# Kernel tuning notes

Hardware: AMD Instinct MI355X
Metric: run time of the kernel (lower is better)

## Reference

```python
import jax, jax.numpy as jnp
import numpy as np

NEG_SLOPE = 0.2


def add_self_loops(edge_index, num_nodes):
    loop = jnp.arange(num_nodes, dtype=edge_index.dtype)
    loops = jnp.stack([loop, loop])  # [2, N]
    return jnp.concatenate([edge_index, loops], axis=1)


def gat_conv(x, edge_index, W, a_src, a_dst, b, concat=True):
    """PyG-style GATConv. a_src/a_dst: [1, H, C]. W: [F_in, H*C]."""
    N = x.shape[0]
    H, C = a_src.shape[1], a_src.shape[2]
    xp = (x @ W).reshape(N, H, C)                       # [N, H, C]
    alpha_src = (xp * a_src).sum(-1)                    # [N, H]
    alpha_dst = (xp * a_dst).sum(-1)                    # [N, H]
    src, dst = edge_index[0], edge_index[1]
    e = alpha_src[src] + alpha_dst[dst]                 # [E, H]
    e = jnp.where(e > 0, e, NEG_SLOPE * e)              # LeakyReLU(0.2)
    # per-destination segment softmax
    m = jax.ops.segment_max(e, dst, num_segments=N)     # [N, H]
    m = jnp.where(jnp.isfinite(m), m, 0.0)
    ez = jnp.exp(e - m[dst])
    s = jax.ops.segment_sum(ez, dst, num_segments=N)    # [N, H]
    alpha = ez / (s[dst] + 1e-16)                       # [E, H]
    msg = xp[src] * alpha[:, :, None]                   # [E, H, C]
    out = jax.ops.segment_sum(msg, dst, num_segments=N) # [N, H, C]
    out = out.reshape(N, H * C) if concat else out.mean(axis=1)
    return out + b


def setup_inputs() -> dict:
    key = jax.random.key(0)
    ks = jax.random.split(key, 16)
    N, F, E, CLS = 100000, 256, 1600000, 10
    x = jax.random.normal(ks[0], (N, F), dtype=jnp.float32)
    edge_index = jax.random.randint(ks[1], (2, E), 0, N, dtype=jnp.int64)

    def glorot(k, shape):
        fan = shape[0] + shape[-1] * (shape[1] if len(shape) == 3 else 1)
        return jax.random.uniform(k, shape, jnp.float32, -1.0, 1.0) * jnp.sqrt(6.0 / fan)

    return {
        "x": x, "edge_index": edge_index,
        "W1": glorot(ks[2], (F, 128)),  "a1s": glorot(ks[3], (1, 8, 16)),
        "a1d": glorot(ks[4], (1, 8, 16)), "b1": jnp.zeros((128,), jnp.float32),
        "W2": glorot(ks[5], (128, 64)), "a2s": glorot(ks[6], (1, 8, 8)),
        "a2d": glorot(ks[7], (1, 8, 8)),  "b2": jnp.zeros((64,), jnp.float32),
        "W3": glorot(ks[8], (64, CLS)), "a3s": glorot(ks[9], (1, 1, CLS)),
        "a3d": glorot(ks[10], (1, 1, CLS)), "b3": jnp.zeros((CLS,), jnp.float32),
    }


def reference(x, edge_index, W1, a1s, a1d, b1, W2, a2s, a2d, b2, W3, a3s, a3d, b3):
    ei = add_self_loops(edge_index, x.shape[0])
    h = jax.nn.elu(gat_conv(x, ei, W1, a1s, a1d, b1))
    h = jax.nn.elu(gat_conv(h, ei, W2, a2s, a2d, b2))
    h = gat_conv(h, ei, W3, a3s, a3d, b3)
    return jax.nn.log_softmax(h, axis=1)
```

## Files before the change

kernel.cpp:

```cpp
#include <hip/hip_runtime.h>
#include <hip/hip_bf16.h>
#include <math.h>


#define LEAKY(v) ((v) > 0.f ? (v) : 0.2f * (v))

typedef __bf16 bf16_t;
typedef __bf16 bf16x8 __attribute__((ext_vector_type(8)));
typedef __bf16 bf16x4 __attribute__((ext_vector_type(4)));
typedef float f32x4 __attribute__((ext_vector_type(4)));
typedef unsigned short u16x8 __attribute__((ext_vector_type(8)));

static __device__ __forceinline__ unsigned short bf_bits(float f) {
    bf16_t b = (bf16_t)f;
    return __builtin_bit_cast(unsigned short, b);
}
static __device__ __forceinline__ float bf_to_f(unsigned short u) {
    return __uint_as_float(((unsigned int)u) << 16);
}
static __device__ __forceinline__ float bperm_f(int byteaddr, float v) {
    return __uint_as_float((unsigned)__builtin_amdgcn_ds_bpermute(byteaddr, (int)__float_as_uint(v)));
}

constexpr int NB_MAX = 400;
constexpr int BCAP = 5120;

__global__ __launch_bounds__(256) void partition_k(
        const int* __restrict__ src, const int* __restrict__ dst, int E, int NB,
        int* __restrict__ bcur, unsigned* __restrict__ staged) {
    __shared__ int hist[NB_MAX];
    __shared__ int bstart[NB_MAX + 1];
    __shared__ int cur[NB_MAX];
    __shared__ int gbase[NB_MAX];
    __shared__ unsigned words[4096];
    __shared__ unsigned short bidl[4096];
    int tid = threadIdx.x;
    int e0 = blockIdx.x * 4096;
    int cnt = E - e0; if (cnt > 4096) cnt = 4096;
    if (cnt <= 0) return;

    for (int b = tid; b < NB; b += 256) hist[b] = 0;
    __syncthreads();
    for (int i = tid; i < cnt; i += 256) atomicAdd(&hist[dst[e0 + i] >> 8], 1);
    __syncthreads();
    if (tid == 0) {
        int run = 0;
        for (int b = 0; b < NB; b++) { bstart[b] = run; run += hist[b]; }
        bstart[NB] = run;
    }
    __syncthreads();
    for (int b = tid; b < NB; b += 256) {
        cur[b] = bstart[b];
        gbase[b] = hist[b] ? atomicAdd(&bcur[b], hist[b]) : 0;
    }
    __syncthreads();
    for (int i = tid; i < cnt; i += 256) {
        int s = src[e0 + i], d = dst[e0 + i];
        int b = d >> 8;
        unsigned w = (unsigned)s | ((unsigned)(d & 255) << 17);
        int p = atomicAdd(&cur[b], 1);
        words[p] = w;
        bidl[p] = (unsigned short)b;
    }
    __syncthreads();
    for (int i = tid; i < cnt; i += 256) {
        int b = bidl[i];
        staged[(size_t)b * BCAP + gbase[b] + (i - bstart[b])] = words[i];
    }
}

__global__ void scan_nb_k(const int* __restrict__ bcur, int* __restrict__ ebase, int NB) {
    int lane = threadIdx.x;
    int CH = (NB + 63) / 64;
    int b0 = lane * CH;
    int v[8]; int s = 0;
#pragma unroll 8
    for (int k = 0; k < CH; k++) { int b = b0 + k; int t = (b < NB) ? bcur[b] : 0; if (k < 8) v[k] = t; s += t; }
    int orig = s;
    for (int off = 1; off < 64; off <<= 1) {
        int t = __shfl_up(s, off, 64);
        if (lane >= off) s += t;
    }
    int run = s - orig;
    for (int k = 0; k < CH; k++) { int b = b0 + k; if (b < NB) { ebase[b] = run; run += v[k]; } }
    if (lane == 63) ebase[NB] = run;
}

__global__ __launch_bounds__(256) void buildcsr_k(
        const unsigned* __restrict__ staged, const int* __restrict__ bcur,
        const int* __restrict__ ebase, int* __restrict__ offs, int* __restrict__ cols,
        int N, int NB) {
    __shared__ int h[256], hs[256], curl[256];
    __shared__ int colsl[BCAP];
    int b = blockIdx.x, tid = threadIdx.x;
    int n0 = b << 8;
    int ecnt = bcur[b];
    int base_g = ebase[b];
    const unsigned* sb = staged + (size_t)b * BCAP;

    h[tid] = 0;
    __syncthreads();
    for (int i = tid; i < ecnt; i += 256) atomicAdd(&h[sb[i] >> 17], 1);
    __syncthreads();
    int val = h[tid];
    hs[tid] = val; __syncthreads();
    for (int off = 1; off < 256; off <<= 1) {
        int t = (tid >= off) ? hs[tid - off] : 0;
        __syncthreads();
        hs[tid] += t;
        __syncthreads();
    }
    int excl = hs[tid] - val;
    curl[tid] = excl;
    if (n0 + tid < N) offs[n0 + tid] = base_g + excl;
    if (b == NB - 1 && tid == 0) offs[N] = base_g + ecnt;
    __syncthreads();
    for (int i = tid; i < ecnt; i += 256) {
        unsigned w = sb[i];
        int p = atomicAdd(&curl[w >> 17], 1);
        colsl[p] = (int)(w & 0x1FFFFu);
    }
    __syncthreads();
    for (int i = tid; i < ecnt; i += 256) cols[base_g + i] = colsl[i];
}

__global__ void prep_w_k(const float* __restrict__ W, short* __restrict__ Bfs,
                         int K, int N, int NT, int total) {
    int idx = blockIdx.x * blockDim.x + threadIdx.x;
    if (idx >= total) return;
    int lane = idx & 63;
    int t = idx >> 6;
    int ntile = t % NT, kstep = t / NT;
    int quad = lane >> 4, nl = lane & 15;
    int n = ntile * 16 + nl;
    bf16_t* dst = (bf16_t*)Bfs + (size_t)idx * 16;
#pragma unroll
    for (int j = 0; j < 8; j++) {
        int k = kstep * 32 + quad * 8 + j;
        float v = W[k * N + n];
        bf16_t h = (bf16_t)v;
        bf16_t l = (bf16_t)(v - (float)h);
        dst[j] = h;
        dst[8 + j] = l;
    }
}

__global__ void prep_w3_k(const float* __restrict__ W, short* __restrict__ Bfs, int Nc) {
    int idx = blockIdx.x * blockDim.x + threadIdx.x;
    if (idx >= 128) return;
    int lane = idx & 63, ks = idx >> 6;
    int quad = lane >> 4, nl = lane & 15;
    bf16_t* dst = (bf16_t*)Bfs + (size_t)idx * 16;
#pragma unroll
    for (int j = 0; j < 8; j++) {
        int k = ks * 32 + quad * 8 + j;
        float v = (nl < Nc) ? W[k * Nc + nl] : 0.f;
        bf16_t h = (bf16_t)v;
        bf16_t l = (bf16_t)(v - (float)h);
        dst[j] = h;
        dst[8 + j] = l;
    }
}

template <int BM, int WMT, int WNT, int NWM, bool ABF16, int CHEAD, int K>
__global__ __launch_bounds__(256, 2) void mfma_gemm_k(
        const void* __restrict__ Av, const short* __restrict__ Bfs,
        unsigned short* __restrict__ Cb,
        const float* __restrict__ a_s, const float* __restrict__ a_d,
        float* __restrict__ out_as, float* __restrict__ out_ad,
        int M, int N, int NT) {
    constexpr int NWN = 4 / NWM;
    constexpr int BN = 16 * WNT * NWN;
    constexpr int KP = K + 8;
    __shared__ __align__(16) bf16_t As_hi[BM * KP];
    __shared__ __align__(16) bf16_t As_lo[ABF16 ? 16 : BM * KP];
    const bf16_t* Bf = (const bf16_t*)Bfs;

    int tid = threadIdx.x;
    int wave = tid >> 6, lane = tid & 63;
    int quad = lane >> 4, l16 = lane & 15;
    int wm = wave % NWM, wn = wave / NWM;
    int row0 = blockIdx.x * BM;
    int ntile0 = blockIdx.y * (BN / 16) + wn * WNT;

    if constexpr (!ABF16) {
        constexpr int CHUNKS = BM * K * 4 / (16 * 256);
        const float* A = (const float*)Av;
        f32x4 tmp[CHUNKS];
#pragma unroll
        for (int c = 0; c < CHUNKS; c++) {
            int ci = c * 256 + tid;
            int fi = ci * 4;
            int row = fi / K, k = fi % K;
            int grow = row0 + row;
            tmp[c] = (f32x4){0.f, 0.f, 0.f, 0.f};
            if (grow < M) tmp[c] = *(const f32x4*)(A + (size_t)grow * K + k);
        }
#pragma unroll
        for (int c = 0; c < CHUNKS; c++) {
            int ci = c * 256 + tid;
            int fi = ci * 4;
            int row = fi / K, k = fi % K;
            bf16x4 h, l;
#pragma unroll
            for (int j = 0; j < 4; j++) {
                bf16_t hh = (bf16_t)tmp[c][j];
                h[j] = hh;
                l[j] = (bf16_t)(tmp[c][j] - (float)hh);
            }
            *(bf16x4*)&As_hi[row * KP + k] = h;
            *(bf16x4*)&As_lo[row * KP + k] = l;
        }
    } else {
        constexpr int CHUNKS = BM * K * 2 / (16 * 256);
        const unsigned short* A = (const unsigned short*)Av;
        u16x8 tmp[CHUNKS];
#pragma unroll
        for (int c = 0; c < CHUNKS; c++) {
            int ci = c * 256 + tid;
            int ei = ci * 8;
            int row = ei / K, k = ei % K;
            int grow = row0 + row;
            tmp[c] = (u16x8){0, 0, 0, 0, 0, 0, 0, 0};
            if (grow < M) tmp[c] = *(const u16x8*)(A + (size_t)grow * K + k);
        }
#pragma unroll
        for (int c = 0; c < CHUNKS; c++) {
            int ci = c * 256 + tid;
            int ei = ci * 8;
            int row = ei / K, k = ei % K;
            *(u16x8*)&As_hi[row * KP + k] = tmp[c];
        }
    }
    __syncthreads();

    f32x4 acc[WMT][WNT];
#pragma unroll
    for (int i = 0; i < WMT; i++)
#pragma unroll
        for (int j = 0; j < WNT; j++) acc[i][j] = (f32x4){0.f, 0.f, 0.f, 0.f};

#pragma unroll
    for (int ks = 0; ks < K / 32; ks++) {
        bf16x8 ah[WMT], al[WMT];
#pragma unroll
        for (int i = 0; i < WMT; i++) {
            int rowl = wm * (WMT * 16) + i * 16 + l16;
            ah[i] = *(const bf16x8*)&As_hi[rowl * KP + ks * 32 + quad * 8];
            if (!ABF16) al[i] = *(const bf16x8*)&As_lo[rowl * KP + ks * 32 + quad * 8];
        }
        bf16x8 bh[WNT], bl[WNT];
#pragma unroll
        for (int j = 0; j < WNT; j++) {
            size_t base = ((size_t)(ks * NT + ntile0 + j) * 64 + lane) * 16;
            bh[j] = *(const bf16x8*)&Bf[base];
            bl[j] = *(const bf16x8*)&Bf[base + 8];
        }
#pragma unroll
        for (int i = 0; i < WMT; i++)
#pragma unroll
            for (int j = 0; j < WNT; j++) {
                acc[i][j] = __builtin_amdgcn_mfma_f32_16x16x32_bf16(ah[i], bh[j], acc[i][j], 0, 0, 0);
                if (!ABF16)
                    acc[i][j] = __builtin_amdgcn_mfma_f32_16x16x32_bf16(al[i], bh[j], acc[i][j], 0, 0, 0);
                acc[i][j] = __builtin_amdgcn_mfma_f32_16x16x32_bf16(ah[i], bl[j], acc[i][j], 0, 0, 0);
            }
    }

#pragma unroll
    for (int i = 0; i < WMT; i++) {
        int rbase = row0 + wm * (WMT * 16) + i * 16 + quad * 4;
#pragma unroll
        for (int j = 0; j < WNT; j++) {
            int gcol = (ntile0 + j) * 16 + l16;
#pragma unroll
            for (int r2 = 0; r2 < 4; r2++) {
                int grow = rbase + r2;
                if (grow < M) Cb[(size_t)grow * N + gcol] = bf_bits(acc[i][j][r2]);
            }
        }
    }

    const int Hh = N / CHEAD;
#pragma unroll
    for (int j = 0; j < WNT; j++) {
        int gcol = (ntile0 + j) * 16 + l16;
        float cs = a_s[gcol], cd = a_d[gcol];
#pragma unroll
        for (int i = 0; i < WMT; i++) {
            float ps[4], pd[4];
#pragma unroll
            for (int r2 = 0; r2 < 4; r2++) {
                ps[r2] = acc[i][j][r2] * cs;
                pd[r2] = acc[i][j][r2] * cd;
            }
#pragma unroll
            for (int off = 1; off < CHEAD; off <<= 1) {
#pragma unroll
                for (int r2 = 0; r2 < 4; r2++) {
                    ps[r2] += __shfl_xor(ps[r2], off, 64);
                    pd[r2] += __shfl_xor(pd[r2], off, 64);
                }
            }
            if ((l16 & (CHEAD - 1)) == 0) {
                int hd = gcol / CHEAD;
                int rb = row0 + wm * (WMT * 16) + i * 16 + quad * 4;
#pragma unroll
                for (int r2 = 0; r2 < 4; r2++) {
                    int grow = rb + r2;
                    if (grow < M) {
                        out_as[(size_t)grow * Hh + hd] = ps[r2];
                        out_ad[(size_t)grow * Hh + hd] = pd[r2];
                    }
                }
            }
        }
    }
}

__global__ __launch_bounds__(256) void gemm3_k(
        const unsigned short* __restrict__ Ab, const short* __restrict__ Bfs,
        unsigned short* __restrict__ Cb,
        const float* __restrict__ a_s, const float* __restrict__ a_d,
        float* __restrict__ out_as, float* __restrict__ out_ad, int M) {
    const bf16_t* Bf = (const bf16_t*)Bfs;
    int tid = threadIdx.x;
    int wave = tid >> 6, lane = tid & 63;
    int quad = lane >> 4, l16 = lane & 15;
    int grow0 = blockIdx.x * 64 + wave * 16;

    bf16x8 bh[2], bl[2];
#pragma unroll
    for (int ks = 0; ks < 2; ks++) {
        size_t base = (size_t)(ks * 64 + lane) * 16;
        bh[ks] = *(const bf16x8*)&Bf[base];
        bl[ks] = *(const bf16x8*)&Bf[base + 8];
    }

    int arow = grow0 + l16; if (arow >= M) arow = M - 1;
    f32x4 acc = (f32x4){0.f, 0.f, 0.f, 0.f};
#pragma unroll
    for (int ks = 0; ks < 2; ks++) {
        bf16x8 a = *(const bf16x8*)(Ab + (size_t)arow * 64 + ks * 32 + quad * 8);
        acc = __builtin_amdgcn_mfma_f32_16x16x32_bf16(a, bh[ks], acc, 0, 0, 0);
        acc = __builtin_amdgcn_mfma_f32_16x16x32_bf16(a, bl[ks], acc, 0, 0, 0);
    }

    bool colv = l16 < 10;
    float cs = colv ? a_s[l16] : 0.f;
    float cd = colv ? a_d[l16] : 0.f;
    float ps[4], pd[4];
#pragma unroll
    for (int r = 0; r < 4; r++) { ps[r] = acc[r] * cs; pd[r] = acc[r] * cd; }
#pragma unroll
    for (int off = 1; off < 16; off <<= 1) {
#pragma unroll
        for (int r = 0; r < 4; r++) {
            ps[r] += __shfl_xor(ps[r], off, 64);
            pd[r] += __shfl_xor(pd[r], off, 64);
        }
    }
#pragma unroll
    for (int r = 0; r < 4; r++) {
        int grow = grow0 + quad * 4 + r;
        if (grow < M) {
            if (colv) Cb[(size_t)grow * 10 + l16] = bf_bits(acc[r]);
            if (l16 == 0) { out_as[grow] = ps[r]; out_ad[grow] = pd[r]; }
        }
    }
}

template <bool DO_ELU>
__global__ void agg16_k(const unsigned short* __restrict__ xpb,
                        const float* __restrict__ asrc, const float* __restrict__ adst,
                        const int* __restrict__ offs, const int* __restrict__ cols,
                        const float* __restrict__ bias, unsigned short* __restrict__ outb,
                        int N) {
    int gtid = blockIdx.x * blockDim.x + threadIdx.x;
    int n = gtid >> 6;
    if (n >= N) return;
    int lane = threadIdx.x & 63;
    int j = lane >> 3, h = lane & 7;
    const int jb = j << 2;
    int start = offs[n], end = offs[n + 1];
    const unsigned* xp32 = (const unsigned*)xpb;

    unsigned uself = xp32[(size_t)n * 64 + lane];
    float ad_l = adst[n * 8 + h];
    float vs = asrc[n * 8 + h] + ad_l;
    vs = LEAKY(vs);

    float m_w = vs;
    float s = (j == 0) ? 1.f : 0.f;
    float m_f = bperm_f(jb, vs);
    float a0 = __uint_as_float(uself << 16);
    float a1 = __uint_as_float(uself & 0xffff0000u);

    for (int c0 = start; c0 < end; c0 += 16) {
        int e0 = c0 + j, e1 = c0 + 8 + j;
        bool ok0 = e0 < end, ok1 = e1 < end;
        int sl0 = ok0 ? cols[e0] : 0;
        int sl1 = ok1 ? cols[e1] : 0;
        unsigned u[16];
#pragma unroll
        for (int t = 0; t < 8; t++) {
            int srcj = __builtin_amdgcn_readlane(sl0, t * 8);
            u[t] = xp32[(size_t)srcj * 64 + lane];
        }
#pragma unroll
        for (int t = 0; t < 8; t++) {
            int srcj = __builtin_amdgcn_readlane(sl1, t * 8);
            u[8 + t] = xp32[(size_t)srcj * 64 + lane];
        }
        float v0 = -1e30f, v1 = -1e30f;
        if (ok0) { v0 = asrc[sl0 * 8 + h] + ad_l; v0 = LEAKY(v0); }
        if (ok1) { v1 = asrc[sl1 * 8 + h] + ad_l; v1 = LEAKY(v1); }
        float cm = fmaxf(v0, v1);
        cm = fmaxf(cm, __shfl_xor(cm, 8, 64));
        cm = fmaxf(cm, __shfl_xor(cm, 16, 64));
        cm = fmaxf(cm, __shfl_xor(cm, 32, 64));
        float mw_new = fmaxf(m_w, cm);
        float w0 = __expf(v0 - mw_new);
        float w1 = __expf(v1 - mw_new);
        s = s * __expf(m_w - mw_new) + w0 + w1;
        m_w = mw_new;
        float cmF = bperm_f(jb, cm);
        float mf_new = fmaxf(m_f, cmF);
        float scF = __expf(m_f - mf_new);
        m_f = mf_new;
        a0 *= scF; a1 *= scF;
        float wl[16];
#pragma unroll
        for (int t = 0; t < 8; t++) wl[t] = bperm_f(jb + t * 32, w0);
#pragma unroll
        for (int t = 0; t < 8; t++) wl[8 + t] = bperm_f(jb + t * 32, w1);
#pragma unroll
        for (int t = 0; t < 16; t++) {
            a0 = fmaf(wl[t], __uint_as_float(u[t] << 16), a0);
            a1 = fmaf(wl[t], __uint_as_float(u[t] & 0xffff0000u), a1);
        }
    }
    s += __shfl_xor(s, 8, 64);
    s += __shfl_xor(s, 16, 64);
    s += __shfl_xor(s, 32, 64);
    float rs = 1.f / (s + 1e-16f);
    float rsF = bperm_f(jb, rs);
    float o0 = a0 * rsF + bias[2 * lane];
    float o1 = a1 * rsF + bias[2 * lane + 1];
    if (DO_ELU) {
        o0 = o0 > 0.f ? o0 : __expf(o0) - 1.f;
        o1 = o1 > 0.f ? o1 : __expf(o1) - 1.f;
    }
    unsigned packed = (unsigned)bf_bits(o0) | ((unsigned)bf_bits(o1) << 16);
    ((unsigned*)outb)[(size_t)n * 64 + lane] = packed;
}

template <bool DO_ELU>
__global__ void agg8c8_k(const unsigned short* __restrict__ xpb,
                         const float* __restrict__ asrc, const float* __restrict__ adst,
                         const int* __restrict__ offs, const int* __restrict__ cols,
                         const float* __restrict__ bias, unsigned short* __restrict__ outb,
                         int N) {
    int gtid = blockIdx.x * blockDim.x + threadIdx.x;
    int n = gtid >> 6;
    if (n >= N) return;
    int lane = threadIdx.x & 63;
    int j = lane >> 3, h = lane & 7;
    int start = offs[n], end = offs[n + 1];
    const unsigned* xp32 = (const unsigned*)xpb;

    int fp = lane & 31;
    int hF = fp >> 2;
    int half = lane >> 5;
    int sbase = half * 32;

    float ad_l = adst[n * 8 + h];
    float vs = asrc[n * 8 + h] + ad_l;
    vs = LEAKY(vs);

    float m_w = vs;
    float s = (j == 0) ? 1.f : 0.f;
    float m_f = bperm_f(hF * 4, vs);
    float a0 = 0.f, a1 = 0.f;
    if (half == 0) {
        unsigned u = xp32[(size_t)n * 32 + fp];
        a0 = __uint_as_float(u << 16);
        a1 = __uint_as_float(u & 0xffff0000u);
    }

    for (int c0 = start; c0 < end; c0 += 16) {
        int e0 = c0 + j, e1 = c0 + 8 + j;
        bool ok0 = e0 < end, ok1 = e1 < end;
        int sl0 = ok0 ? cols[e0] : 0;
        int sl1 = ok1 ? cols[e1] : 0;
        int sv[8];
#pragma unroll
        for (int t = 0; t < 4; t++) sv[t] = __builtin_amdgcn_ds_bpermute(sbase + t * 64, sl0);
#pragma unroll
        for (int t = 0; t < 4; t++) sv[4 + t] = __builtin_amdgcn_ds_bpermute(sbase + t * 64, sl1);
        unsigned u[8];
#pragma unroll
        for (int t = 0; t < 8; t++) u[t] = xp32[(size_t)sv[t] * 32 + fp];
        float v0 = -1e30f, v1 = -1e30f;
        if (ok0) { v0 = asrc[sl0 * 8 + h] + ad_l; v0 = LEAKY(v0); }
        if (ok1) { v1 = asrc[sl1 * 8 + h] + ad_l; v1 = LEAKY(v1); }
        float cm = fmaxf(v0, v1);
        cm = fmaxf(cm, __shfl_xor(cm, 8, 64));
        cm = fmaxf(cm, __shfl_xor(cm, 16, 64));
        cm = fmaxf(cm, __shfl_xor(cm, 32, 64));
        float mw_new = fmaxf(m_w, cm);
        float w0 = __expf(v0 - mw_new);
        float w1 = __expf(v1 - mw_new);
        s = s * __expf(m_w - mw_new) + w0 + w1;
        m_w = mw_new;
        float cmF = bperm_f(hF * 4, cm);
        float mf_new = fmaxf(m_f, cmF);
        float scF = __expf(m_f - mf_new);
        m_f = mf_new;
        a0 *= scF; a1 *= scF;
        float wl[8];
#pragma unroll
        for (int t = 0; t < 4; t++) wl[t] = bperm_f(sbase + hF * 4 + t * 64, w0);
#pragma unroll
        for (int t = 0; t < 4; t++) wl[4 + t] = bperm_f(sbase + hF * 4 + t * 64, w1);
#pragma unroll
        for (int t = 0; t < 8; t++) {
            a0 = fmaf(wl[t], __uint_as_float(u[t] << 16), a0);
            a1 = fmaf(wl[t], __uint_as_float(u[t] & 0xffff0000u), a1);
        }
    }
    s += __shfl_xor(s, 8, 64);
    s += __shfl_xor(s, 16, 64);
    s += __shfl_xor(s, 32, 64);
    float rs = 1.f / (s + 1e-16f);
    float rsF = bperm_f(hF * 4, rs);
    a0 += __shfl_xor(a0, 32, 64);
    a1 += __shfl_xor(a1, 32, 64);
    if (half == 0) {
        float o0 = a0 * rsF + bias[2 * fp];
        float o1 = a1 * rsF + bias[2 * fp + 1];
        if (DO_ELU) {
            o0 = o0 > 0.f ? o0 : __expf(o0) - 1.f;
            o1 = o1 > 0.f ? o1 : __expf(o1) - 1.f;
        }
        unsigned packed = (unsigned)bf_bits(o0) | ((unsigned)bf_bits(o1) << 16);
        ((unsigned*)outb)[(size_t)n * 32 + fp] = packed;
    }
}

__global__ void agg1h_k(const unsigned short* __restrict__ xpb,
                        const float* __restrict__ asrc, const float* __restrict__ adst,
                        const int* __restrict__ offs, const int* __restrict__ cols,
                        const float* __restrict__ bias, float* __restrict__ out, int N) {
    int gtid = blockIdx.x * blockDim.x + threadIdx.x;
    int n = gtid >> 6;
    if (n >= N) return;
    int lane = threadIdx.x & 63;
    int start = offs[n], end = offs[n + 1];
    float ad = adst[n];
    float vs = asrc[n] + ad;
    vs = LEAKY(vs);

    float m, s;
    if (lane == 0) { m = vs; s = 1.f; } else { m = -1e30f; s = 0.f; }
    for (int e = start + lane; e < end; e += 64) {
        float v = asrc[cols[e]] + ad;
        v = LEAKY(v);
        float mo = fmaxf(m, v);
        s = s * __expf(m - mo) + __expf(v - mo);
        m = mo;
    }
#pragma unroll
    for (int off = 1; off <= 32; off <<= 1) {
        float mo = __shfl_xor(m, off, 64);
        float so = __shfl_xor(s, off, 64);
        float mn = fmaxf(m, mo);
        s = s * __expf(m - mn) + so * __expf(mo - mn);
        m = mn;
    }
    float rs = 1.f / (s + 1e-16f);
    float wself = __expf(vs - m) * rs;

    int j = lane / 10, c = lane - j * 10;
    float acc = 0.f;
    if (j == 0) acc = wself * bf_to_f(xpb[(size_t)n * 10 + c]);
    for (int c0 = start; c0 < end; c0 += 6) {
        int e = c0 + j;
        if (j < 6 && e < end) {
            int src = cols[e];
            float v = asrc[src] + ad;
            v = LEAKY(v);
            float w = __expf(v - m) * rs;
            acc = fmaf(w, bf_to_f(xpb[(size_t)src * 10 + c]), acc);
        }
    }
    float tot = acc;
#pragma unroll
    for (int k = 1; k < 6; k++) tot += __shfl(acc, lane + 10 * k, 64);

    float z = tot + bias[lane < 10 ? lane : 0];
    float mx = -1e30f;
#pragma unroll
    for (int k = 0; k < 10; k++) mx = fmaxf(mx, __shfl(z, k, 64));
    float se = 0.f;
#pragma unroll
    for (int k = 0; k < 10; k++) se += __expf(__shfl(z, k, 64) - mx);
    if (lane < 10) out[(size_t)n * 10 + lane] = z - (__logf(se) + mx);
}


static inline size_t alignup(size_t x) { return (x + 255) & ~(size_t)255; }

extern "C" void kernel_launch(void* const* d_in, const int* in_sizes, int n_in,
                              void* d_out, int out_size, void* d_ws, size_t ws_size,
                              hipStream_t stream) {
    const float* x   = (const float*)d_in[0];
    const int*   ei  = (const int*)d_in[1];
    const float* W1  = (const float*)d_in[2];
    const float* a1s = (const float*)d_in[3];
    const float* a1d = (const float*)d_in[4];
    const float* b1  = (const float*)d_in[5];
    const float* W2  = (const float*)d_in[6];
    const float* a2s = (const float*)d_in[7];
    const float* a2d = (const float*)d_in[8];
    const float* b2  = (const float*)d_in[9];
    const float* W3  = (const float*)d_in[10];
    const float* a3s = (const float*)d_in[11];
    const float* a3d = (const float*)d_in[12];
    const float* b3  = (const float*)d_in[13];
    float* out = (float*)d_out;

    const int N = in_sizes[0] / 256;
    const int E = in_sizes[1] / 2;
    const int* src = ei;
    const int* dst = ei + E;
    const int NB = (N + 255) >> 8;

    char* p = (char*)d_ws;
    int* offs    = (int*)p; p += alignup(sizeof(int) * (size_t)(N + 1));
    int* bcur    = (int*)p; p += alignup(sizeof(int) * (size_t)(NB_MAX + 1));
    int* ebase   = (int*)p; p += alignup(sizeof(int) * (size_t)(NB_MAX + 1));
    int* cols    = (int*)p; p += alignup(sizeof(int) * (size_t)E);
    unsigned short* xpb   = (unsigned short*)p; p += alignup(2 * (size_t)N * 128);
    unsigned short* hbufb = (unsigned short*)p; p += alignup(2 * (size_t)N * 128);
    float* xp    = (float*)p; p += alignup(sizeof(float) * (size_t)N * 128);
    float* as_   = (float*)p; p += alignup(sizeof(float) * (size_t)N * 8);
    float* ad_   = (float*)p; p += alignup(sizeof(float) * (size_t)N * 8);
    short* Bf1   = (short*)p; p += alignup(sizeof(short) * 8 * 8 * 64 * 16);
    short* Bf2   = (short*)p; p += alignup(sizeof(short) * 4 * 4 * 64 * 16);
    short* Bf3   = (short*)p; p += alignup(sizeof(short) * 2 * 1 * 64 * 16);
    unsigned* staged = (unsigned*)xp;

    const int TB = 256;

    hipMemsetAsync(bcur, 0, sizeof(int) * (size_t)(NB + 1), stream);
    partition_k<<<(E + 4095) / 4096, 256, 0, stream>>>(src, dst, E, NB, bcur, staged);
    scan_nb_k<<<1, 64, 0, stream>>>(bcur, ebase, NB);
    buildcsr_k<<<NB, 256, 0, stream>>>(staged, bcur, ebase, offs, cols, N, NB);

    prep_w_k<<<(4096 + TB - 1) / TB, TB, 0, stream>>>(W1, Bf1, 256, 128, 8, 4096);
    prep_w_k<<<(1024 + TB - 1) / TB, TB, 0, stream>>>(W2, Bf2, 128, 64, 4, 1024);
    prep_w3_k<<<1, 128, 0, stream>>>(W3, Bf3, 10);

    mfma_gemm_k<64, 4, 2, 1, false, 16, 256><<<dim3((N + 63) / 64, 1), 256, 0, stream>>>(
        x, Bf1, xpb, a1s, a1d, as_, ad_, N, 128, 8);
    agg16_k<true><<<(N * 64 + TB - 1) / TB, TB, 0, stream>>>(
        xpb, as_, ad_, offs, cols, b1, hbufb, N);

    mfma_gemm_k<64, 4, 1, 1, true, 8, 128><<<dim3((N + 63) / 64, 1), 256, 0, stream>>>(
        hbufb, Bf2, xpb, a2s, a2d, as_, ad_, N, 64, 4);
    agg8c8_k<true><<<(N * 64 + TB - 1) / TB, TB, 0, stream>>>(
        xpb, as_, ad_, offs, cols, b2, hbufb, N);

    gemm3_k<<<(N + 63) / 64, 256, 0, stream>>>(
        hbufb, Bf3, xpb, a3s, a3d, as_, ad_, N);
    agg1h_k<<<(N * 64 + TB - 1) / TB, TB, 0, stream>>>(
        xpb, as_, ad_, offs, cols, b3, out, N);
}
```

Measured before the change: 509.6 us.

## Fuse small prep kernels, parallelize partition scan, stage GEMM epilogue through LDS

The partition kernel's serial bucket prefix scan now runs as a 64-lane wave scan. The separate scan_nb kernel is removed, and each buildcsr block computes its own base by summing the preceding bucket counts. The three weight-prep kernels are merged into one launch. The GEMM epilogue now writes accumulators into shared memory reused from the A tile. From there it computes the attention dot products per row and head and stores packed bf16 pairs with coalesced writes, replacing the scattered 16-bit stores and shuffle reductions. These changes cut launch count and serial work and improve store coalescing, at the cost of extra LDS traffic and barriers.

```diff
diff --git a/kernel.cpp b/kernel.cpp
--- a/kernel.cpp
+++ b/kernel.cpp
@@ -43,10 +43,21 @@
     __syncthreads();
     for (int i = tid; i < cnt; i += 256) atomicAdd(&hist[dst[e0 + i] >> 8], 1);
     __syncthreads();
-    if (tid == 0) {
+    if (tid < 64) {
+        int lane = tid;
         int run = 0;
-        for (int b = 0; b < NB; b++) { bstart[b] = run; run += hist[b]; }
-        bstart[NB] = run;
+        for (int b0 = 0; b0 < NB; b0 += 64) {
+            int bb = b0 + lane;
+            int v = (bb < NB) ? hist[bb] : 0;
+            int sc = v;
+            for (int off = 1; off < 64; off <<= 1) {
+                int t2 = __shfl_up(sc, off, 64);
+                if (lane >= off) sc += t2;
+            }
+            if (bb < NB) bstart[bb] = run + sc - v;
+            run += __shfl(sc, 63, 64);
+        }
+        if (lane == 0) bstart[NB] = run;
     }
     __syncthreads();
     for (int b = tid; b < NB; b += 256) {
@@ -69,37 +80,27 @@
     }
 }
 
-__global__ void scan_nb_k(const int* __restrict__ bcur, int* __restrict__ ebase, int NB) {
-    int lane = threadIdx.x;
-    int CH = (NB + 63) / 64;
-    int b0 = lane * CH;
-    int v[8]; int s = 0;
-#pragma unroll 8
-    for (int k = 0; k < CH; k++) { int b = b0 + k; int t = (b < NB) ? bcur[b] : 0; if (k < 8) v[k] = t; s += t; }
-    int orig = s;
-    for (int off = 1; off < 64; off <<= 1) {
-        int t = __shfl_up(s, off, 64);
-        if (lane >= off) s += t;
-    }
-    int run = s - orig;
-    for (int k = 0; k < CH; k++) { int b = b0 + k; if (b < NB) { ebase[b] = run; run += v[k]; } }
-    if (lane == 63) ebase[NB] = run;
-}
-
 __global__ __launch_bounds__(256) void buildcsr_k(
         const unsigned* __restrict__ staged, const int* __restrict__ bcur,
-        const int* __restrict__ ebase, int* __restrict__ offs, int* __restrict__ cols,
+        int* __restrict__ offs, int* __restrict__ cols,
         int N, int NB) {
     __shared__ int h[256], hs[256], curl[256];
     __shared__ int colsl[BCAP];
+    __shared__ int base_s;
     int b = blockIdx.x, tid = threadIdx.x;
     int n0 = b << 8;
     int ecnt = bcur[b];
-    int base_g = ebase[b];
     const unsigned* sb = staged + (size_t)b * BCAP;
 
     h[tid] = 0;
-    __syncthreads();
+    if (tid < 64) {
+        int acc2 = 0;
+        for (int i = tid; i < b; i += 64) acc2 += bcur[i];
+        for (int off = 1; off < 64; off <<= 1) acc2 += __shfl_xor(acc2, off, 64);
+        if (tid == 0) base_s = acc2;
+    }
+    __syncthreads();
+    int base_g = base_s;
     for (int i = tid; i < ecnt; i += 256) atomicAdd(&h[sb[i] >> 17], 1);
     __syncthreads();
     int val = h[tid];
@@ -124,10 +125,9 @@
     for (int i = tid; i < ecnt; i += 256) cols[base_g + i] = colsl[i];
 }
 
-__global__ void prep_w_k(const float* __restrict__ W, short* __restrict__ Bfs,
-                         int K, int N, int NT, int total) {
-    int idx = blockIdx.x * blockDim.x + threadIdx.x;
-    if (idx >= total) return;
+static __device__ __forceinline__ void prep_w_dev(
+        const float* __restrict__ W, short* __restrict__ Bfs,
+        int K, int N, int NT, int idx) {
     int lane = idx & 63;
     int t = idx >> 6;
     int ntile = t % NT, kstep = t / NT;
@@ -144,10 +144,8 @@
         dst[8 + j] = l;
     }
 }
-
-__global__ void prep_w3_k(const float* __restrict__ W, short* __restrict__ Bfs, int Nc) {
-    int idx = blockIdx.x * blockDim.x + threadIdx.x;
-    if (idx >= 128) return;
+static __device__ __forceinline__ void prep_w3_dev(
+        const float* __restrict__ W, short* __restrict__ Bfs, int Nc, int idx) {
     int lane = idx & 63, ks = idx >> 6;
     int quad = lane >> 4, nl = lane & 15;
     bf16_t* dst = (bf16_t*)Bfs + (size_t)idx * 16;
@@ -160,6 +158,14 @@
         dst[j] = h;
         dst[8 + j] = l;
     }
+}
+__global__ void prep_all_k(const float* __restrict__ W1, const float* __restrict__ W2,
+                           const float* __restrict__ W3, short* __restrict__ Bf1,
+                           short* __restrict__ Bf2, short* __restrict__ Bf3) {
+    int idx = blockIdx.x * blockDim.x + threadIdx.x;
+    if (idx < 4096) prep_w_dev(W1, Bf1, 256, 128, 8, idx);
+    else if (idx < 5120) prep_w_dev(W2, Bf2, 128, 64, 4, idx - 4096);
+    else if (idx < 5248) prep_w3_dev(W3, Bf3, 10, idx - 5120);
 }
 
 template <int BM, int WMT, int WNT, int NWM, bool ABF16, int CHEAD, int K>
@@ -172,8 +178,14 @@
     constexpr int NWN = 4 / NWM;
     constexpr int BN = 16 * WNT * NWN;
     constexpr int KP = K + 8;
-    __shared__ __align__(16) bf16_t As_hi[BM * KP];
-    __shared__ __align__(16) bf16_t As_lo[ABF16 ? 16 : BM * KP];
+    constexpr int BNP = BN + 2;
+    constexpr size_t ASZ = (size_t)BM * KP * 2 * (ABF16 ? 1 : 2);
+    constexpr size_t CSZ = (size_t)BM * BNP * 4;
+    constexpr size_t SMEM = ASZ > CSZ ? ASZ : CSZ;
+    __shared__ __align__(16) char smem[SMEM];
+    bf16_t* As_hi = (bf16_t*)smem;
+    bf16_t* As_lo = As_hi + (ABF16 ? 0 : (size_t)BM * KP);
+    float* Ct = (float*)smem;
     const bf16_t* Bf = (const bf16_t*)Bfs;
 
     int tid = threadIdx.x;
@@ -267,54 +279,57 @@
             }
     }
 
+    __syncthreads();
 #pragma unroll
     for (int i = 0; i < WMT; i++) {
-        int rbase = row0 + wm * (WMT * 16) + i * 16 + quad * 4;
+        int rbase = wm * (WMT * 16) + i * 16 + quad * 4;
 #pragma unroll
         for (int j = 0; j < WNT; j++) {
-            int gcol = (ntile0 + j) * 16 + l16;
-#pragma unroll
-            for (int r2 = 0; r2 < 4; r2++) {
-                int grow = rbase + r2;
-                if (grow < M) Cb[(size_t)grow * N + gcol] = bf_bits(acc[i][j][r2]);
+            int lcol = (wn * WNT + j) * 16 + l16;
+#pragma unroll
+            for (int r2 = 0; r2 < 4; r2++)
+                Ct[(size_t)(rbase + r2) * BNP + lcol] = acc[i][j][r2];
+        }
+    }
+    __syncthreads();
+
+    constexpr int HB = BN / CHEAD;
+    const int colbase = blockIdx.y * BN;
+    const int Hh = N / CHEAD;
+#pragma unroll
+    for (int o = 0; o < (BM * HB + 255) / 256; o++) {
+        int idx = o * 256 + tid;
+        if (idx < BM * HB) {
+            int row = idx & (BM - 1);
+            int hd = idx / BM;
+            const float* crow = Ct + (size_t)row * BNP + hd * CHEAD;
+            float ss = 0.f, sd = 0.f;
+#pragma unroll
+            for (int c = 0; c < CHEAD; c++) {
+                float v = crow[c];
+                ss = fmaf(v, a_s[colbase + hd * CHEAD + c], ss);
+                sd = fmaf(v, a_d[colbase + hd * CHEAD + c], sd);
             }
-        }
-    }
-
-    const int Hh = N / CHEAD;
-#pragma unroll
-    for (int j = 0; j < WNT; j++) {
-        int gcol = (ntile0 + j) * 16 + l16;
-        float cs = a_s[gcol], cd = a_d[gcol];
-#pragma unroll
-        for (int i = 0; i < WMT; i++) {
-            float ps[4], pd[4];
-#pragma unroll
-            for (int r2 = 0; r2 < 4; r2++) {
-                ps[r2] = acc[i][j][r2] * cs;
-                pd[r2] = acc[i][j][r2] * cd;
+            int grow = row0 + row;
+            if (grow < M) {
+                out_as[(size_t)grow * Hh + blockIdx.y * HB + hd] = ss;
+                out_ad[(size_t)grow * Hh + blockIdx.y * HB + hd] = sd;
             }
-#pragma unroll
-            for (int off = 1; off < CHEAD; off <<= 1) {
-#pragma unroll
-                for (int r2 = 0; r2 < 4; r2++) {
-                    ps[r2] += __shfl_xor(ps[r2], off, 64);
-                    pd[r2] += __shfl_xor(pd[r2], off, 64);
-                }
-            }
-            if ((l16 & (CHEAD - 1)) == 0) {
-                int hd = gcol / CHEAD;
-                int rb = row0 + wm * (WMT * 16) + i * 16 + quad * 4;
-#pragma unroll
-                for (int r2 = 0; r2 < 4; r2++) {
-                    int grow = rb + r2;
-                    if (grow < M) {
-                        out_as[(size_t)grow * Hh + hd] = ps[r2];
-                        out_ad[(size_t)grow * Hh + hd] = pd[r2];
-                    }
-                }
-            }
-        }
+        }
+    }
+
+    constexpr int CU2 = BM * BN / 2;
+#pragma unroll
+    for (int o = 0; o < CU2 / 256; o++) {
+        int idx = o * 256 + tid;
+        int row = idx / (BN / 2);
+        int uc = idx - row * (BN / 2);
+        float v0 = Ct[(size_t)row * BNP + uc * 2];
+        float v1 = Ct[(size_t)row * BNP + uc * 2 + 1];
+        unsigned pk = (unsigned)bf_bits(v0) | ((unsigned)bf_bits(v1) << 16);
+        int grow = row0 + row;
+        if (grow < M)
+            ((unsigned*)Cb)[((size_t)grow * N + colbase) / 2 + uc] = pk;
     }
 }
 
@@ -639,7 +654,6 @@
     char* p = (char*)d_ws;
     int* offs    = (int*)p; p += alignup(sizeof(int) * (size_t)(N + 1));
     int* bcur    = (int*)p; p += alignup(sizeof(int) * (size_t)(NB_MAX + 1));
-    int* ebase   = (int*)p; p += alignup(sizeof(int) * (size_t)(NB_MAX + 1));
     int* cols    = (int*)p; p += alignup(sizeof(int) * (size_t)E);
     unsigned short* xpb   = (unsigned short*)p; p += alignup(2 * (size_t)N * 128);
     unsigned short* hbufb = (unsigned short*)p; p += alignup(2 * (size_t)N * 128);
@@ -655,12 +669,9 @@
 
     hipMemsetAsync(bcur, 0, sizeof(int) * (size_t)(NB + 1), stream);
     partition_k<<<(E + 4095) / 4096, 256, 0, stream>>>(src, dst, E, NB, bcur, staged);
-    scan_nb_k<<<1, 64, 0, stream>>>(bcur, ebase, NB);
-    buildcsr_k<<<NB, 256, 0, stream>>>(staged, bcur, ebase, offs, cols, N, NB);
-
-    prep_w_k<<<(4096 + TB - 1) / TB, TB, 0, stream>>>(W1, Bf1, 256, 128, 8, 4096);
-    prep_w_k<<<(1024 + TB - 1) / TB, TB, 0, stream>>>(W2, Bf2, 128, 64, 4, 1024);
-    prep_w3_k<<<1, 128, 0, stream>>>(W3, Bf3, 10);
+    buildcsr_k<<<NB, 256, 0, stream>>>(staged, bcur, offs, cols, N, NB);
+
+    prep_all_k<<<(5248 + TB - 1) / TB, TB, 0, stream>>>(W1, W2, W3, Bf1, Bf2, Bf3);
 
     mfma_gemm_k<64, 4, 2, 1, false, 16, 256><<<dim3((N + 63) / 64, 1), 256, 0, stream>>>(
         x, Bf1, xpb, a1s, a1d, as_, ad_, N, 128, 8);
```

Measured after the change: 477.2 us. -6.4%, faster.
